# Performance work log

Hardware: AMD Instinct MI355X
Metric: run time of the kernel (lower is better)

## Reference

```python
import jax, jax.numpy as jnp
import numpy as np

B, D, C = 2048, 512, 50000
MARGIN = 0.3
SCALE = 30.0
EPS = 1e-12


def setup_inputs() -> dict:
    key = jax.random.key(0)
    k1, k2, k3 = jax.random.split(key, 3)
    embeddings = jax.random.normal(k1, (B, D), dtype=jnp.float32)
    labels = jax.random.randint(k2, (B,), 0, C, dtype=jnp.int64)
    # Xavier-uniform init for weight (num_classes, in_features)
    limit = float(np.sqrt(6.0 / (C + D)))
    weight = jax.random.uniform(k3, (C, D), dtype=jnp.float32, minval=-limit, maxval=limit)
    return {"embeddings": embeddings, "labels": labels, "weight": weight}


def _l2_normalize(x, axis):
    # Matches torch F.normalize(p=2, eps=1e-12): x / max(||x||, eps)
    norm = jnp.sqrt(jnp.sum(x * x, axis=axis, keepdims=True))
    return x / jnp.maximum(norm, EPS)


def reference(embeddings, labels, weight):
    emb_n = _l2_normalize(embeddings, axis=1)            # (B, D)
    w_n = _l2_normalize(weight, axis=1)                  # (C, D)
    cos = jnp.einsum("bd,cd->bc", emb_n, w_n)            # (B, C)
    # margin subtract at label index (avoid dense one-hot materialization)
    rows = jnp.arange(cos.shape[0])
    phi = cos.at[rows, labels].add(-MARGIN)
    logits = phi * SCALE
    # cross-entropy with mean reduction
    logp = jax.nn.log_softmax(logits, axis=-1)
    nll = -jnp.take_along_axis(logp, labels[:, None], axis=-1)[:, 0]
    return jnp.mean(nll)
```

## Files before the change

kernel.cpp:

```cpp
#include <hip/hip_runtime.h>
#include <hip/hip_bf16.h>
#include <math.h>
#include <stdint.h>


#define B_ROWS    2048
#define D_DIM     512
#define C_CLASSES 50000
#define C_PAD     50176
#define NCHUNK    112
#define CH_COLS   448
#define NSTRIP    14
#define ARC_MARGIN 0.3f
#define ARC_SCALE  30.0f
#define ARC_EPS    1e-12f
#define K_LOG2E_S  43.2808512f

#define OFF_WQ    0u
#define OFF_EMBQ  25690112u
#define OFF_WINV  26738688u
#define OFF_EINV  26938688u
#define OFF_PART  26946880u

typedef __attribute__((ext_vector_type(8))) int   i32x8;
typedef __attribute__((ext_vector_type(4))) int   i32x4;
typedef __attribute__((ext_vector_type(4))) float f32x4;

typedef __attribute__((address_space(1))) const unsigned int g_u32;
typedef __attribute__((address_space(3))) unsigned int       l_u32;

__device__ __forceinline__ void gload_lds16(const void* g, void* l) {
    g_u32* gp = (g_u32*)(uintptr_t)g;
    l_u32* lp = (l_u32*)(uintptr_t)l;
    __builtin_amdgcn_global_load_lds(gp, lp, 16, 0, 0);
}

__global__ __launch_bounds__(256) void k_prep(const float* __restrict__ emb,
                                              const float* __restrict__ weight,
                                              uint8_t* __restrict__ embq,
                                              uint8_t* __restrict__ wq,
                                              float* __restrict__ einv,
                                              float* __restrict__ winv,
                                              float* __restrict__ out) {
    if (blockIdx.x == 0 && threadIdx.x == 0) out[0] = 0.f;
    int wave = blockIdx.x * (blockDim.x >> 6) + (threadIdx.x >> 6);
    int lane = threadIdx.x & 63;
    int g0   = wave << 2;

    const float* src;
    uint8_t* dst;
    float* invout;
    if (g0 >= C_PAD) {
        int row = g0 - C_PAD;
        src = emb + (size_t)row * D_DIM;
        dst = embq + (size_t)row * D_DIM;
        invout = einv + row;
    } else if (g0 >= C_CLASSES) {
        int2 z = make_int2(0, 0);
        #pragma unroll
        for (int r = 0; r < 4; ++r)
            *(int2*)(wq + (size_t)(g0 + r) * D_DIM + lane * 8) = z;
        return;
    } else {
        src = weight + (size_t)g0 * D_DIM;
        dst = wq + (size_t)g0 * D_DIM;
        invout = winv + g0;
    }

    const float4* r4 = (const float4*)src;
    float4 v[8];
    #pragma unroll
    for (int r = 0; r < 4; ++r) {
        v[2 * r]     = r4[r * 128 + lane * 2];
        v[2 * r + 1] = r4[r * 128 + lane * 2 + 1];
    }

    #pragma unroll
    for (int r = 0; r < 4; ++r) {
        float4 v0 = v[2 * r], v1 = v[2 * r + 1];
        float s = v0.x*v0.x + v0.y*v0.y + v0.z*v0.z + v0.w*v0.w
                + v1.x*v1.x + v1.y*v1.y + v1.z*v1.z + v1.w*v1.w;
        #pragma unroll
        for (int off = 32; off; off >>= 1) s += __shfl_xor(s, off);
        float rn = 1.0f / fmaxf(sqrtf(s), ARC_EPS);
        if (lane == 0) invout[r] = rn;
        int p0 = __builtin_amdgcn_cvt_pk_fp8_f32(v0.x * rn, v0.y * rn, 0, false);
        p0     = __builtin_amdgcn_cvt_pk_fp8_f32(v0.z * rn, v0.w * rn, p0, true);
        int p1 = __builtin_amdgcn_cvt_pk_fp8_f32(v1.x * rn, v1.y * rn, 0, false);
        p1     = __builtin_amdgcn_cvt_pk_fp8_f32(v1.z * rn, v1.w * rn, p1, true);
        *(int2*)(dst + (size_t)r * D_DIM + lane * 8) = make_int2(p0, p1);
    }
}

struct TrueT  { static constexpr bool value = true;  };
struct FalseT { static constexpr bool value = false; };

__global__ __launch_bounds__(256) void k_gemm(const uint8_t* __restrict__ embq,
                                              const uint8_t* __restrict__ wq,
                                              float* __restrict__ partials) {
    __shared__ __align__(16) uint8_t Bs[2][16384];

    const int tid  = threadIdx.x;
    const int w    = tid >> 6;
    const int lane = tid & 63;
    const int c    = lane & 15;
    const int q    = lane >> 4;

    const int id  = blockIdx.x;
    const int xcd = id & 7;
    const int s   = id >> 3;
    const int ci  = s % 14;
    const int rb  = s / 14;
    const int chunk = xcd * 14 + ci;
    const int b0 = rb * 128;
    const int n0 = chunk * CH_COLS;

    const int r0 = b0 + w * 32;
    i32x8 afA[4], afB[4];
    #pragma unroll
    for (int kt = 0; kt < 4; ++kt) {
        const uint8_t* pa = embq + (size_t)(r0 + c) * D_DIM + kt * 128 + q * 32;
        const uint8_t* pb = embq + (size_t)(r0 + 16 + c) * D_DIM + kt * 128 + q * 32;
        i32x4 alo = *(const i32x4*)pa;
        i32x4 ahi = *(const i32x4*)(pa + 16);
        i32x4 blo = *(const i32x4*)pb;
        i32x4 bhi = *(const i32x4*)(pb + 16);
        afA[kt] = (i32x8){alo[0], alo[1], alo[2], alo[3], ahi[0], ahi[1], ahi[2], ahi[3]};
        afB[kt] = (i32x8){blo[0], blo[1], blo[2], blo[3], bhi[0], bhi[1], bhi[2], bhi[3]};
    }

    const int srow = c;
    const int skc  = q;
    auto stage = [&](uint8_t* dst, int st) {
        const uint8_t* base = wq + (size_t)(n0 + st * 32) * D_DIM;
        #pragma unroll
        for (int t = 0; t < 4; ++t) {
            const int p  = w * 4 + t;
            const int cb = p >> 3;
            const int h  = p & 7;
            gload_lds16(base + (size_t)(cb * 16 + srow) * D_DIM + (h * 4 + skc) * 16,
                        dst + cb * 8192 + h * 1024);
        }
    };

    f32x4 rs0 = (f32x4){0.f, 0.f, 0.f, 0.f};
    f32x4 rs1 = (f32x4){0.f, 0.f, 0.f, 0.f};

    auto compute = [&](const uint8_t* buf, int st, auto maskTag) {
        constexpr bool MASK = decltype(maskTag)::value;
        #pragma unroll
        for (int cb = 0; cb < 2; ++cb) {
            f32x4 a0 = (f32x4){0.f, 0.f, 0.f, 0.f};
            f32x4 a1 = (f32x4){0.f, 0.f, 0.f, 0.f};
            #pragma unroll
            for (int kt = 0; kt < 4; ++kt) {
                const uint8_t* p = buf + cb * 8192 + (kt * 8 + 2 * q) * 256 + c * 16;
                i32x4 lo = *(const i32x4*)p;
                i32x4 hi = *(const i32x4*)(p + 256);
                i32x8 bf = (i32x8){lo[0], lo[1], lo[2], lo[3],
                                   hi[0], hi[1], hi[2], hi[3]};
                a0 = __builtin_amdgcn_mfma_scale_f32_16x16x128_f8f6f4(
                        afA[kt], bf, a0, 0, 0, 0, 127, 0, 127);
                a1 = __builtin_amdgcn_mfma_scale_f32_16x16x128_f8f6f4(
                        afB[kt], bf, a1, 0, 0, 0, 127, 0, 127);
            }
            bool pad = false;
            if (MASK) pad = (n0 + st * 32 + cb * 16 + c) >= C_CLASSES;
            #pragma unroll
            for (int reg = 0; reg < 4; ++reg) {
                float t0 = __builtin_amdgcn_exp2f(fmaf(a0[reg], K_LOG2E_S, -K_LOG2E_S));
                float t1 = __builtin_amdgcn_exp2f(fmaf(a1[reg], K_LOG2E_S, -K_LOG2E_S));
                if (MASK && pad) { t0 = 0.f; t1 = 0.f; }
                rs0[reg] += t0;
                rs1[reg] += t1;
            }
        }
    };

    auto run = [&](auto maskTag) {
        stage(&Bs[0][0], 0);
        __syncthreads();
        #pragma unroll 1
        for (int st = 0; st < NSTRIP; st += 2) {
            stage(&Bs[1][0], st + 1);
            compute(&Bs[0][0], st, maskTag);
            __syncthreads();
            if (st + 2 < NSTRIP) stage(&Bs[0][0], st + 2);
            compute(&Bs[1][0], st + 1, maskTag);
            __syncthreads();
        }
    };
    if (chunk == NCHUNK - 1) run(TrueT{}); else run(FalseT{});

    #pragma unroll
    for (int off = 1; off < 16; off <<= 1) {
        #pragma unroll
        for (int reg = 0; reg < 4; ++reg) {
            rs0[reg] += __shfl_xor(rs0[reg], off);
            rs1[reg] += __shfl_xor(rs1[reg], off);
        }
    }
    if (c == 0) {
        #pragma unroll
        for (int reg = 0; reg < 4; ++reg) {
            partials[(size_t)(r0 + q * 4 + reg) * NCHUNK + chunk]      = rs0[reg];
            partials[(size_t)(r0 + 16 + q * 4 + reg) * NCHUNK + chunk] = rs1[reg];
        }
    }
}

__global__ __launch_bounds__(256) void k_fin(const float* __restrict__ emb,
                                             const float* __restrict__ weight,
                                             const float* __restrict__ einv,
                                             const float* __restrict__ winv,
                                             const int* __restrict__ labels,
                                             const float* __restrict__ partials,
                                             float* __restrict__ out) {
    __shared__ float s_dot[2], s_ls[2];
    int widx = threadIdx.x >> 6;
    int lane = threadIdx.x & 63;
    int rloc = widx & 1;
    int role = widx >> 1;
    int b    = blockIdx.x * 2 + rloc;

    if (role == 0) {
        int label = labels[b];
        const float4* e  = (const float4*)(emb + (size_t)b * D_DIM);
        const float4* wt = (const float4*)(weight + (size_t)label * D_DIM);
        float4 e0 = e[lane],  e1 = e[lane + 64];
        float4 w0 = wt[lane], w1 = wt[lane + 64];
        float dot = e0.x*w0.x + e0.y*w0.y + e0.z*w0.z + e0.w*w0.w
                  + e1.x*w1.x + e1.y*w1.y + e1.z*w1.z + e1.w*w1.w;
        #pragma unroll
        for (int off = 32; off; off >>= 1) dot += __shfl_xor(dot, off);
        if (lane == 0) s_dot[rloc] = dot;
    } else {
        float p0 = partials[(size_t)b * NCHUNK + lane];
        float p1 = (lane + 64 < NCHUNK) ? partials[(size_t)b * NCHUNK + lane + 64] : 0.f;
        float ls = p0 + p1;
        #pragma unroll
        for (int off = 32; off; off >>= 1) ls += __shfl_xor(ls, off);
        if (lane == 0) s_ls[rloc] = ls;
    }
    __syncthreads();

    if (threadIdx.x < 2) {
        int r = threadIdx.x;
        int b2 = blockIdx.x * 2 + r;
        int label = labels[b2];
        float cosv   = s_dot[r] * einv[b2] * winv[label];
        float l_orig = ARC_SCALE * cosv;
        float l_adj  = ARC_SCALE * (cosv - ARC_MARGIN);
        float s_adj = s_ls[r] - __expf(l_orig - ARC_SCALE) + __expf(l_adj - ARC_SCALE);
        float v = ARC_SCALE + logf(s_adj) - l_adj;
        atomicAdd(out, v * (1.0f / (float)B_ROWS));
    }
}

extern "C" void kernel_launch(void* const* d_in, const int* in_sizes, int n_in,
                              void* d_out, int out_size, void* d_ws, size_t ws_size,
                              hipStream_t stream) {
    const float* emb    = (const float*)d_in[0];
    const int*   labels = (const int*)d_in[1];
    const float* weight = (const float*)d_in[2];
    float* out = (float*)d_out;

    char* ws = (char*)d_ws;
    uint8_t* wq    = (uint8_t*)(ws + OFF_WQ);
    uint8_t* embq  = (uint8_t*)(ws + OFF_EMBQ);
    float* winv     = (float*)(ws + OFF_WINV);
    float* einv     = (float*)(ws + OFF_EINV);
    float* partials = (float*)(ws + OFF_PART);

    k_prep<<<(C_PAD + B_ROWS) / 16, 256, 0, stream>>>(emb, weight, embq, wq,
                                                      einv, winv, out);

    k_gemm<<<1792, 256, 0, stream>>>(embq, wq, partials);

    k_fin<<<B_ROWS / 2, 256, 0, stream>>>(emb, weight, einv, winv, labels,
                                          partials, out);
}
```

Baseline: 240.9 us.

## Replace per-row atomics with two-stage reduction and widen prep/fin per-wave work

k_prep now has each wave handle 8 rows instead of 4, which halves the grid and keeps more loads in flight per wave. k_fin now gives each wave two complete rows and does both the label dot and the partial-sum reduction in that wave, so 8 rows are processed per block. Each block writes one partial sum, and a new single-block k_sum kernel produces the mean. This removes 2048 same-address atomics and the zero-init in k_prep, at the cost of one extra kernel launch and higher register use in k_prep.

New measurement: 234.2 us. 1.03x faster.

```diff
diff --git a/kernel.cpp b/kernel.cpp
--- a/kernel.cpp
+++ b/kernel.cpp
@@ -21,6 +21,7 @@
 #define OFF_WINV  26738688u
 #define OFF_EINV  26938688u
 #define OFF_PART  26946880u
+#define OFF_FINP  27864384u
 
 typedef __attribute__((ext_vector_type(8))) int   i32x8;
 typedef __attribute__((ext_vector_type(4))) int   i32x4;
@@ -42,10 +43,9 @@
                                               float* __restrict__ einv,
                                               float* __restrict__ winv,
                                               float* __restrict__ out) {
-    if (blockIdx.x == 0 && threadIdx.x == 0) out[0] = 0.f;
     int wave = blockIdx.x * (blockDim.x >> 6) + (threadIdx.x >> 6);
     int lane = threadIdx.x & 63;
-    int g0   = wave << 2;
+    int g0   = wave << 3;
 
     const float* src;
     uint8_t* dst;
@@ -58,7 +58,7 @@
     } else if (g0 >= C_CLASSES) {
         int2 z = make_int2(0, 0);
         #pragma unroll
-        for (int r = 0; r < 4; ++r)
+        for (int r = 0; r < 8; ++r)
             *(int2*)(wq + (size_t)(g0 + r) * D_DIM + lane * 8) = z;
         return;
     } else {
@@ -68,15 +68,15 @@
     }
 
     const float4* r4 = (const float4*)src;
-    float4 v[8];
-    #pragma unroll
-    for (int r = 0; r < 4; ++r) {
+    float4 v[16];
+    #pragma unroll
+    for (int r = 0; r < 8; ++r) {
         v[2 * r]     = r4[r * 128 + lane * 2];
         v[2 * r + 1] = r4[r * 128 + lane * 2 + 1];
     }
 
     #pragma unroll
-    for (int r = 0; r < 4; ++r) {
+    for (int r = 0; r < 8; ++r) {
         float4 v0 = v[2 * r], v1 = v[2 * r + 1];
         float s = v0.x*v0.x + v0.y*v0.y + v0.z*v0.z + v0.w*v0.w
                 + v1.x*v1.x + v1.y*v1.y + v1.z*v1.z + v1.w*v1.w;
@@ -215,46 +215,65 @@
                                              const float* __restrict__ winv,
                                              const int* __restrict__ labels,
                                              const float* __restrict__ partials,
+                                             float* __restrict__ finpart) {
+    __shared__ float sm[8];
+    int w    = threadIdx.x >> 6;
+    int lane = threadIdx.x & 63;
+    int b0   = blockIdx.x * 8 + w * 2;
+
+    int lab[2] = {labels[b0], labels[b0 + 1]};
+    float4 e0[2], e1[2], w0[2], w1[2];
+    float p0[2], p1[2];
+    #pragma unroll
+    for (int r = 0; r < 2; ++r) {
+        const float4* e  = (const float4*)(emb + (size_t)(b0 + r) * D_DIM);
+        const float4* wt = (const float4*)(weight + (size_t)lab[r] * D_DIM);
+        e0[r] = e[lane];  e1[r] = e[lane + 64];
+        w0[r] = wt[lane]; w1[r] = wt[lane + 64];
+        p0[r] = partials[(size_t)(b0 + r) * NCHUNK + lane];
+        p1[r] = (lane + 64 < NCHUNK)
+              ? partials[(size_t)(b0 + r) * NCHUNK + lane + 64] : 0.f;
+    }
+
+    #pragma unroll
+    for (int r = 0; r < 2; ++r) {
+        float dot = e0[r].x*w0[r].x + e0[r].y*w0[r].y + e0[r].z*w0[r].z + e0[r].w*w0[r].w
+                  + e1[r].x*w1[r].x + e1[r].y*w1[r].y + e1[r].z*w1[r].z + e1[r].w*w1[r].w;
+        float ls = p0[r] + p1[r];
+        #pragma unroll
+        for (int off = 32; off; off >>= 1) {
+            dot += __shfl_xor(dot, off);
+            ls  += __shfl_xor(ls, off);
+        }
+        if (lane == 0) {
+            int b = b0 + r;
+            float cosv   = dot * einv[b] * winv[lab[r]];
+            float l_orig = ARC_SCALE * cosv;
+            float l_adj  = ARC_SCALE * (cosv - ARC_MARGIN);
+            float s_adj = ls - __expf(l_orig - ARC_SCALE) + __expf(l_adj - ARC_SCALE);
+            sm[w * 2 + r] = ARC_SCALE + logf(s_adj) - l_adj;
+        }
+    }
+    __syncthreads();
+    if (threadIdx.x == 0) {
+        float t = 0.f;
+        #pragma unroll
+        for (int i = 0; i < 8; ++i) t += sm[i];
+        finpart[blockIdx.x] = t;
+    }
+}
+
+__global__ __launch_bounds__(256) void k_sum(const float* __restrict__ finpart,
                                              float* __restrict__ out) {
-    __shared__ float s_dot[2], s_ls[2];
-    int widx = threadIdx.x >> 6;
-    int lane = threadIdx.x & 63;
-    int rloc = widx & 1;
-    int role = widx >> 1;
-    int b    = blockIdx.x * 2 + rloc;
-
-    if (role == 0) {
-        int label = labels[b];
-        const float4* e  = (const float4*)(emb + (size_t)b * D_DIM);
-        const float4* wt = (const float4*)(weight + (size_t)label * D_DIM);
-        float4 e0 = e[lane],  e1 = e[lane + 64];
-        float4 w0 = wt[lane], w1 = wt[lane + 64];
-        float dot = e0.x*w0.x + e0.y*w0.y + e0.z*w0.z + e0.w*w0.w
-                  + e1.x*w1.x + e1.y*w1.y + e1.z*w1.z + e1.w*w1.w;
-        #pragma unroll
-        for (int off = 32; off; off >>= 1) dot += __shfl_xor(dot, off);
-        if (lane == 0) s_dot[rloc] = dot;
-    } else {
-        float p0 = partials[(size_t)b * NCHUNK + lane];
-        float p1 = (lane + 64 < NCHUNK) ? partials[(size_t)b * NCHUNK + lane + 64] : 0.f;
-        float ls = p0 + p1;
-        #pragma unroll
-        for (int off = 32; off; off >>= 1) ls += __shfl_xor(ls, off);
-        if (lane == 0) s_ls[rloc] = ls;
-    }
+    __shared__ float sm[4];
+    int w = threadIdx.x >> 6, lane = threadIdx.x & 63;
+    float v = finpart[threadIdx.x];
+    #pragma unroll
+    for (int off = 32; off; off >>= 1) v += __shfl_xor(v, off);
+    if (lane == 0) sm[w] = v;
     __syncthreads();
-
-    if (threadIdx.x < 2) {
-        int r = threadIdx.x;
-        int b2 = blockIdx.x * 2 + r;
-        int label = labels[b2];
-        float cosv   = s_dot[r] * einv[b2] * winv[label];
-        float l_orig = ARC_SCALE * cosv;
-        float l_adj  = ARC_SCALE * (cosv - ARC_MARGIN);
-        float s_adj = s_ls[r] - __expf(l_orig - ARC_SCALE) + __expf(l_adj - ARC_SCALE);
-        float v = ARC_SCALE + logf(s_adj) - l_adj;
-        atomicAdd(out, v * (1.0f / (float)B_ROWS));
-    }
+    if (threadIdx.x == 0)
+        out[0] = (sm[0] + sm[1] + sm[2] + sm[3]) * (1.0f / (float)B_ROWS);
 }
 
 extern "C" void kernel_launch(void* const* d_in, const int* in_sizes, int n_in,
@@ -271,12 +290,14 @@
     float* winv     = (float*)(ws + OFF_WINV);
     float* einv     = (float*)(ws + OFF_EINV);
     float* partials = (float*)(ws + OFF_PART);
-
-    k_prep<<<(C_PAD + B_ROWS) / 16, 256, 0, stream>>>(emb, weight, embq, wq,
+    float* finpart  = (float*)(ws + OFF_FINP);
+
+    k_prep<<<(C_PAD + B_ROWS) / 32, 256, 0, stream>>>(emb, weight, embq, wq,
                                                       einv, winv, out);
 
     k_gemm<<<1792, 256, 0, stream>>>(embq, wq, partials);
 
-    k_fin<<<B_ROWS / 2, 256, 0, stream>>>(emb, weight, einv, winv, labels,
-                                          partials, out);
-}
+    k_fin<<<B_ROWS / 8, 256, 0, stream>>>(emb, weight, einv, winv, labels,
+                                          partials, finpart);
+    k_sum<<<1, 256, 0, stream>>>(finpart, out);
+}
```
